# Optimization experiments

Measured on AMD Instinct MI355X. Metric: run time of the kernel, lower is better.

The kernel has to match this reference:

```python
import jax, jax.numpy as jnp
import numpy as np


def setup_inputs() -> dict:
    key = jax.random.key(0)
    kq, kk, kv = jax.random.split(key, 3)
    B, L, S, H, E = 2, 2048, 2048, 16, 64
    queries = jax.random.normal(kq, (B, L, H, E), dtype=jnp.float32)
    keys = jax.random.normal(kk, (B, S, H, E), dtype=jnp.float32)
    values = jax.random.normal(kv, (B, S, H, E), dtype=jnp.float32)
    # TriangularCausalMask: True strictly above the diagonal (positions to mask)
    causal = jnp.triu(jnp.ones((L, S), dtype=jnp.bool_), k=1)
    attn_mask = jnp.broadcast_to(causal[None, None, :, :], (B, 1, L, S))
    return {"queries": queries, "keys": keys, "values": values, "attn_mask": attn_mask}


def reference(queries, keys, values, attn_mask):
    # queries: [B,L,H,E], keys/values: [B,S,H,E], attn_mask: [B,1,L,S] bool
    E = queries.shape[-1]
    scale = 1.0 / jnp.sqrt(jnp.asarray(E, dtype=queries.dtype))
    scores = jnp.einsum('blhe,bshe->bhls', queries, keys)      # [B,H,L,S]
    scores = jnp.where(attn_mask, -jnp.inf, scores)
    A = jax.nn.softmax(scale * scores, axis=-1)                # dropout is identity in eval
    V = jnp.einsum('bhls,bshd->blhd', A, values)               # [B,L,H,D]
    return V, A
```

## Files before the change

kernel.cpp:

```cpp
#include <hip/hip_runtime.h>
#include <hip/hip_bf16.h>


#define B_ 2
#define L_ 2048
#define S_ 2048
#define H_ 16
#define E_ 64
#define HE 1024
#define KP 72
#define PP 68

typedef __attribute__((ext_vector_type(8))) __bf16 bfrag;
typedef __attribute__((ext_vector_type(4))) float f32x4;

__device__ __forceinline__ unsigned short f2bu(float x) {
    __bf16 b = (__bf16)x;
    return __builtin_bit_cast(unsigned short, b);
}

__global__ __launch_bounds__(256, 2)
void fullattn_kernel(const float* __restrict__ Qg,
                     const float* __restrict__ Kg,
                     const float* __restrict__ Vg,
                     float* __restrict__ Vout,
                     float* __restrict__ Aout)
{
    __shared__ __align__(16) __bf16 Ks[64 * KP];
    __shared__ __align__(16) __bf16 Vt[64 * KP];
    __shared__ __align__(16) float  Pw[4][16 * PP];

    const int tid  = threadIdx.x;
    const int wave = tid >> 6;
    const int lane = tid & 63;
    const int ln   = lane & 15;
    const int quad = lane >> 4;
    const int lq   = quad * 4;

    const int qt = blockIdx.x;
    const int bh = blockIdx.y;
    const int b  = bh >> 4;
    const int h  = bh & 15;

    const int q0  = qt * 64;
    const int q0w = q0 + wave * 16;

    const float* qbase = Qg + ((size_t)b * L_ * H_ + h) * E_;
    const float* kbase = Kg + ((size_t)b * S_ * H_ + h) * E_;
    const float* vbase = Vg + ((size_t)b * S_ * H_ + h) * E_;
    float* arow0 = Aout + (size_t)bh * L_ * S_;

    bfrag qf[2];
    {
        const float* qr = qbase + (size_t)(q0w + ln) * HE;
        #pragma unroll
        for (int kc = 0; kc < 2; ++kc) {
            const float* p = qr + kc * 32 + quad * 8;
            float4 a0 = *(const float4*)(p);
            float4 a1 = *(const float4*)(p + 4);
            bfrag f;
            f[0] = (__bf16)(a0.x * 0.125f); f[1] = (__bf16)(a0.y * 0.125f);
            f[2] = (__bf16)(a0.z * 0.125f); f[3] = (__bf16)(a0.w * 0.125f);
            f[4] = (__bf16)(a1.x * 0.125f); f[5] = (__bf16)(a1.y * 0.125f);
            f[6] = (__bf16)(a1.z * 0.125f); f[7] = (__bf16)(a1.w * 0.125f);
            qf[kc] = f;
        }
    }

    const int r  = tid >> 2;
    const int c0 = tid & 3;

    float lsum[4] = {0.f, 0.f, 0.f, 0.f};
    for (int st = 0; st <= qt; ++st) {
        const int s0 = st * 64;
        __syncthreads();
        {
            const float* kr = kbase + (size_t)(s0 + r) * HE;
            #pragma unroll
            for (int i = 0; i < 4; ++i) {
                int f4 = c0 + i * 4;
                float4 kv = *(const float4*)(kr + f4 * 4);
                ushort4 kb;
                kb.x = f2bu(kv.x); kb.y = f2bu(kv.y);
                kb.z = f2bu(kv.z); kb.w = f2bu(kv.w);
                *(ushort4*)&Ks[r * KP + f4 * 4] = kb;
            }
        }
        __syncthreads();
        #pragma unroll
        for (int nc = 0; nc < 4; ++nc) {
            f32x4 acc = {0.f, 0.f, 0.f, 0.f};
            #pragma unroll
            for (int kc = 0; kc < 2; ++kc) {
                bfrag bk = *(const bfrag*)&Ks[(nc * 16 + ln) * KP + kc * 32 + quad * 8];
                acc = __builtin_amdgcn_mfma_f32_16x16x32_bf16(qf[kc], bk, acc, 0, 0, 0);
            }
            const int s_abs = s0 + nc * 16 + ln;
            #pragma unroll
            for (int rg = 0; rg < 4; ++rg) {
                const int q_abs = q0w + lq + rg;
                float e = (s_abs <= q_abs) ? __expf(acc[rg]) : 0.0f;
                lsum[rg] += e;
            }
        }
    }

    float inv_l[4];
    #pragma unroll
    for (int rg = 0; rg < 4; ++rg) {
        float v = lsum[rg];
        v += __shfl_xor(v, 1);
        v += __shfl_xor(v, 2);
        v += __shfl_xor(v, 4);
        v += __shfl_xor(v, 8);
        inv_l[rg] = 1.0f / v;
    }

    f32x4 oacc[4];
    #pragma unroll
    for (int dc = 0; dc < 4; ++dc) {
        f32x4 z = {0.f, 0.f, 0.f, 0.f};
        oacc[dc] = z;
    }

    const int wr = lane >> 2;
    const int wc = (lane & 3) * 4;

    for (int st = 0; st <= qt; ++st) {
        const int s0 = st * 64;
        __syncthreads();
        {
            const float* kr = kbase + (size_t)(s0 + r) * HE;
            const float* vr = vbase + (size_t)(s0 + r) * HE;
            #pragma unroll
            for (int i = 0; i < 4; ++i) {
                int f4 = c0 + i * 4;
                float4 kv = *(const float4*)(kr + f4 * 4);
                float4 vv = *(const float4*)(vr + f4 * 4);
                ushort4 kb;
                kb.x = f2bu(kv.x); kb.y = f2bu(kv.y);
                kb.z = f2bu(kv.z); kb.w = f2bu(kv.w);
                *(ushort4*)&Ks[r * KP + f4 * 4] = kb;
                const int d0 = f4 * 4;
                Vt[(d0 + 0) * KP + r] = (__bf16)vv.x;
                Vt[(d0 + 1) * KP + r] = (__bf16)vv.y;
                Vt[(d0 + 2) * KP + r] = (__bf16)vv.z;
                Vt[(d0 + 3) * KP + r] = (__bf16)vv.w;
            }
        }
        __syncthreads();

        #pragma unroll
        for (int nc = 0; nc < 4; ++nc) {
            f32x4 acc = {0.f, 0.f, 0.f, 0.f};
            #pragma unroll
            for (int kc = 0; kc < 2; ++kc) {
                bfrag bk = *(const bfrag*)&Ks[(nc * 16 + ln) * KP + kc * 32 + quad * 8];
                acc = __builtin_amdgcn_mfma_f32_16x16x32_bf16(qf[kc], bk, acc, 0, 0, 0);
            }
            const int s_abs = s0 + nc * 16 + ln;
            #pragma unroll
            for (int rg = 0; rg < 4; ++rg) {
                const int q_abs = q0w + lq + rg;
                float e = (s_abs <= q_abs) ? __expf(acc[rg]) : 0.0f;
                Pw[wave][(lq + rg) * PP + nc * 16 + ln] = e * inv_l[rg];
            }
        }

        bfrag af[2];
        #pragma unroll
        for (int kc = 0; kc < 2; ++kc) {
            const float* pp = &Pw[wave][ln * PP + kc * 32 + quad * 8];
            float4 p0 = *(const float4*)pp;
            float4 p1 = *(const float4*)(pp + 4);
            bfrag f;
            f[0] = (__bf16)p0.x; f[1] = (__bf16)p0.y;
            f[2] = (__bf16)p0.z; f[3] = (__bf16)p0.w;
            f[4] = (__bf16)p1.x; f[5] = (__bf16)p1.y;
            f[6] = (__bf16)p1.z; f[7] = (__bf16)p1.w;
            af[kc] = f;
        }

        #pragma unroll
        for (int dc = 0; dc < 4; ++dc) {
            #pragma unroll
            for (int kc = 0; kc < 2; ++kc) {
                bfrag bv = *(const bfrag*)&Vt[(dc * 16 + ln) * KP + kc * 32 + quad * 8];
                oacc[dc] = __builtin_amdgcn_mfma_f32_16x16x32_bf16(af[kc], bv, oacc[dc], 0, 0, 0);
            }
        }

        float* ar = arow0 + (size_t)(q0w + wr) * S_ + s0;
        #pragma unroll
        for (int c4 = 0; c4 < 4; ++c4) {
            float4 v4 = *(const float4*)&Pw[wave][wr * PP + wc + c4 * 16];
            *(float4*)(ar + wc + c4 * 16) = v4;
        }
    }

    {
        const float4 z4 = {0.f, 0.f, 0.f, 0.f};
        for (int st = qt + 1; st < S_ / 64; ++st) {
            float* ar = arow0 + (size_t)(q0w + wr) * S_ + st * 64;
            #pragma unroll
            for (int c4 = 0; c4 < 4; ++c4)
                *(float4*)(ar + wc + c4 * 16) = z4;
        }
    }

    #pragma unroll
    for (int rg = 0; rg < 4; ++rg) {
        float* vr = Vout + ((size_t)(b * L_ + q0w + lq + rg) * H_ + h) * E_;
        #pragma unroll
        for (int dc = 0; dc < 4; ++dc)
            vr[dc * 16 + ln] = oacc[dc][rg];
    }
}

extern "C" void kernel_launch(void* const* d_in, const int* in_sizes, int n_in,
                              void* d_out, int out_size, void* d_ws, size_t ws_size,
                              hipStream_t stream) {
    const float* Q = (const float*)d_in[0];
    const float* K = (const float*)d_in[1];
    const float* V = (const float*)d_in[2];
    float* out  = (float*)d_out;
    float* Vo   = out;
    float* Ao   = out + (size_t)B_ * L_ * H_ * E_;
    dim3 grid(L_ / 64, B_ * H_);
    fullattn_kernel<<<grid, 256, 0, stream>>>(Q, K, V, Vo, Ao);
}
```

Before: 729.2 us.

## Split rowsum into separate kernel, register-prefetch K/V tiles, bf16 P staging

Moves the first pass (row sums of exp scores) into its own kernel that writes inverse normalizers to workspace, and the main kernel reads them. Both kernels now prefetch the next K/V tile into registers while computing the current one, and occupancy hints go from 2 to 4 blocks. P is staged in shared memory as bf16, and the A matrix is written straight from registers as scalar stores instead of float4 stores through shared memory. This trades an extra launch, a workspace round trip and less coalesced A writes for more overlap and occupancy.

```diff
diff --git a/kernel.cpp b/kernel.cpp
--- a/kernel.cpp
+++ b/kernel.cpp
@@ -9,7 +9,7 @@
 #define E_ 64
 #define HE 1024
 #define KP 72
-#define PP 68
+#define PWP 72
 
 typedef __attribute__((ext_vector_type(8))) __bf16 bfrag;
 typedef __attribute__((ext_vector_type(4))) float f32x4;
@@ -19,16 +19,12 @@
     return __builtin_bit_cast(unsigned short, b);
 }
 
-__global__ __launch_bounds__(256, 2)
-void fullattn_kernel(const float* __restrict__ Qg,
-                     const float* __restrict__ Kg,
-                     const float* __restrict__ Vg,
-                     float* __restrict__ Vout,
-                     float* __restrict__ Aout)
+__global__ __launch_bounds__(256, 4)
+void rowsum_kernel(const float* __restrict__ Qg,
+                   const float* __restrict__ Kg,
+                   float* __restrict__ invL)
 {
     __shared__ __align__(16) __bf16 Ks[64 * KP];
-    __shared__ __align__(16) __bf16 Vt[64 * KP];
-    __shared__ __align__(16) float  Pw[4][16 * PP];
 
     const int tid  = threadIdx.x;
     const int wave = tid >> 6;
@@ -41,14 +37,10 @@
     const int bh = blockIdx.y;
     const int b  = bh >> 4;
     const int h  = bh & 15;
-
-    const int q0  = qt * 64;
-    const int q0w = q0 + wave * 16;
+    const int q0w = qt * 64 + wave * 16;
 
     const float* qbase = Qg + ((size_t)b * L_ * H_ + h) * E_;
     const float* kbase = Kg + ((size_t)b * S_ * H_ + h) * E_;
-    const float* vbase = Vg + ((size_t)b * S_ * H_ + h) * E_;
-    float* arow0 = Aout + (size_t)bh * L_ * S_;
 
     bfrag qf[2];
     {
@@ -70,23 +62,30 @@
     const int r  = tid >> 2;
     const int c0 = tid & 3;
 
+    float4 kv[4];
+    {
+        const float* kr = kbase + (size_t)r * HE;
+        #pragma unroll
+        for (int i = 0; i < 4; ++i) kv[i] = *(const float4*)(kr + (c0 + i * 4) * 4);
+    }
+
     float lsum[4] = {0.f, 0.f, 0.f, 0.f};
     for (int st = 0; st <= qt; ++st) {
+        __syncthreads();
+        #pragma unroll
+        for (int i = 0; i < 4; ++i) {
+            ushort4 kb;
+            kb.x = f2bu(kv[i].x); kb.y = f2bu(kv[i].y);
+            kb.z = f2bu(kv[i].z); kb.w = f2bu(kv[i].w);
+            *(ushort4*)&Ks[r * KP + (c0 + i * 4) * 4] = kb;
+        }
+        __syncthreads();
+        if (st < qt) {
+            const float* kr = kbase + (size_t)((st + 1) * 64 + r) * HE;
+            #pragma unroll
+            for (int i = 0; i < 4; ++i) kv[i] = *(const float4*)(kr + (c0 + i * 4) * 4);
+        }
         const int s0 = st * 64;
-        __syncthreads();
-        {
-            const float* kr = kbase + (size_t)(s0 + r) * HE;
-            #pragma unroll
-            for (int i = 0; i < 4; ++i) {
-                int f4 = c0 + i * 4;
-                float4 kv = *(const float4*)(kr + f4 * 4);
-                ushort4 kb;
-                kb.x = f2bu(kv.x); kb.y = f2bu(kv.y);
-                kb.z = f2bu(kv.z); kb.w = f2bu(kv.w);
-                *(ushort4*)&Ks[r * KP + f4 * 4] = kb;
-            }
-        }
-        __syncthreads();
         #pragma unroll
         for (int nc = 0; nc < 4; ++nc) {
             f32x4 acc = {0.f, 0.f, 0.f, 0.f};
@@ -99,13 +98,11 @@
             #pragma unroll
             for (int rg = 0; rg < 4; ++rg) {
                 const int q_abs = q0w + lq + rg;
-                float e = (s_abs <= q_abs) ? __expf(acc[rg]) : 0.0f;
-                lsum[rg] += e;
-            }
-        }
-    }
-
-    float inv_l[4];
+                lsum[rg] += (s_abs <= q_abs) ? __expf(acc[rg]) : 0.f;
+            }
+        }
+    }
+
     #pragma unroll
     for (int rg = 0; rg < 4; ++rg) {
         float v = lsum[rg];
@@ -113,8 +110,61 @@
         v += __shfl_xor(v, 2);
         v += __shfl_xor(v, 4);
         v += __shfl_xor(v, 8);
-        inv_l[rg] = 1.0f / v;
-    }
+        if (ln == 0) invL[(size_t)bh * L_ + q0w + lq + rg] = 1.0f / v;
+    }
+}
+
+__global__ __launch_bounds__(256, 4)
+void fullattn_kernel(const float* __restrict__ Qg,
+                     const float* __restrict__ Kg,
+                     const float* __restrict__ Vg,
+                     const float* __restrict__ invL,
+                     float* __restrict__ Vout,
+                     float* __restrict__ Aout)
+{
+    __shared__ __align__(16) __bf16 Ks[64 * KP];
+    __shared__ __align__(16) __bf16 Vt[64 * KP];
+    __shared__ __align__(16) __bf16 Pwb[4][16 * PWP];
+
+    const int tid  = threadIdx.x;
+    const int wave = tid >> 6;
+    const int lane = tid & 63;
+    const int ln   = lane & 15;
+    const int quad = lane >> 4;
+    const int lq   = quad * 4;
+
+    const int qt = blockIdx.x;
+    const int bh = blockIdx.y;
+    const int b  = bh >> 4;
+    const int h  = bh & 15;
+    const int q0w = qt * 64 + wave * 16;
+
+    const float* qbase = Qg + ((size_t)b * L_ * H_ + h) * E_;
+    const float* kbase = Kg + ((size_t)b * S_ * H_ + h) * E_;
+    const float* vbase = Vg + ((size_t)b * S_ * H_ + h) * E_;
+    float* arow0 = Aout + (size_t)bh * L_ * S_;
+
+    bfrag qf[2];
+    {
+        const float* qr = qbase + (size_t)(q0w + ln) * HE;
+        #pragma unroll
+        for (int kc = 0; kc < 2; ++kc) {
+            const float* p = qr + kc * 32 + quad * 8;
+            float4 a0 = *(const float4*)(p);
+            float4 a1 = *(const float4*)(p + 4);
+            bfrag f;
+            f[0] = (__bf16)(a0.x * 0.125f); f[1] = (__bf16)(a0.y * 0.125f);
+            f[2] = (__bf16)(a0.z * 0.125f); f[3] = (__bf16)(a0.w * 0.125f);
+            f[4] = (__bf16)(a1.x * 0.125f); f[5] = (__bf16)(a1.y * 0.125f);
+            f[6] = (__bf16)(a1.z * 0.125f); f[7] = (__bf16)(a1.w * 0.125f);
+            qf[kc] = f;
+        }
+    }
+
+    float inv_l[4];
+    #pragma unroll
+    for (int rg = 0; rg < 4; ++rg)
+        inv_l[rg] = invL[(size_t)bh * L_ + q0w + lq + rg];
 
     f32x4 oacc[4];
     #pragma unroll
@@ -123,32 +173,51 @@
         oacc[dc] = z;
     }
 
-    const int wr = lane >> 2;
-    const int wc = (lane & 3) * 4;
+    const int r  = tid >> 2;
+    const int c0 = tid & 3;
+
+    float4 kv[4], vv[4];
+    {
+        const float* kr = kbase + (size_t)r * HE;
+        const float* vr = vbase + (size_t)r * HE;
+        #pragma unroll
+        for (int i = 0; i < 4; ++i) {
+            kv[i] = *(const float4*)(kr + (c0 + i * 4) * 4);
+            vv[i] = *(const float4*)(vr + (c0 + i * 4) * 4);
+        }
+    }
+
+    float* arp[4];
+    #pragma unroll
+    for (int rg = 0; rg < 4; ++rg)
+        arp[rg] = arow0 + (size_t)(q0w + lq + rg) * S_ + ln;
 
     for (int st = 0; st <= qt; ++st) {
         const int s0 = st * 64;
         __syncthreads();
-        {
-            const float* kr = kbase + (size_t)(s0 + r) * HE;
-            const float* vr = vbase + (size_t)(s0 + r) * HE;
+        #pragma unroll
+        for (int i = 0; i < 4; ++i) {
+            const int f4 = c0 + i * 4;
+            ushort4 kb;
+            kb.x = f2bu(kv[i].x); kb.y = f2bu(kv[i].y);
+            kb.z = f2bu(kv[i].z); kb.w = f2bu(kv[i].w);
+            *(ushort4*)&Ks[r * KP + f4 * 4] = kb;
+            const int d0 = f4 * 4;
+            Vt[(d0 + 0) * KP + r] = (__bf16)vv[i].x;
+            Vt[(d0 + 1) * KP + r] = (__bf16)vv[i].y;
+            Vt[(d0 + 2) * KP + r] = (__bf16)vv[i].z;
+            Vt[(d0 + 3) * KP + r] = (__bf16)vv[i].w;
+        }
+        __syncthreads();
+        if (st < qt) {
+            const float* kr = kbase + (size_t)((st + 1) * 64 + r) * HE;
+            const float* vr = vbase + (size_t)((st + 1) * 64 + r) * HE;
             #pragma unroll
             for (int i = 0; i < 4; ++i) {
-                int f4 = c0 + i * 4;
-                float4 kv = *(const float4*)(kr + f4 * 4);
-                float4 vv = *(const float4*)(vr + f4 * 4);
-                ushort4 kb;
-                kb.x = f2bu(kv.x); kb.y = f2bu(kv.y);
-                kb.z = f2bu(kv.z); kb.w = f2bu(kv.w);
-                *(ushort4*)&Ks[r * KP + f4 * 4] = kb;
-                const int d0 = f4 * 4;
-                Vt[(d0 + 0) * KP + r] = (__bf16)vv.x;
-                Vt[(d0 + 1) * KP + r] = (__bf16)vv.y;
-                Vt[(d0 + 2) * KP + r] = (__bf16)vv.z;
-                Vt[(d0 + 3) * KP + r] = (__bf16)vv.w;
-            }
-        }
-        __syncthreads();
+                kv[i] = *(const float4*)(kr + (c0 + i * 4) * 4);
+                vv[i] = *(const float4*)(vr + (c0 + i * 4) * 4);
+            }
+        }
 
         #pragma unroll
         for (int nc = 0; nc < 4; ++nc) {
@@ -162,24 +231,17 @@
             #pragma unroll
             for (int rg = 0; rg < 4; ++rg) {
                 const int q_abs = q0w + lq + rg;
-                float e = (s_abs <= q_abs) ? __expf(acc[rg]) : 0.0f;
-                Pw[wave][(lq + rg) * PP + nc * 16 + ln] = e * inv_l[rg];
+                float e = (s_abs <= q_abs) ? __expf(acc[rg]) : 0.f;
+                float p = e * inv_l[rg];
+                arp[rg][s0 + nc * 16] = p;
+                Pwb[wave][(lq + rg) * PWP + nc * 16 + ln] = (__bf16)p;
             }
         }
 
         bfrag af[2];
         #pragma unroll
-        for (int kc = 0; kc < 2; ++kc) {
-            const float* pp = &Pw[wave][ln * PP + kc * 32 + quad * 8];
-            float4 p0 = *(const float4*)pp;
-            float4 p1 = *(const float4*)(pp + 4);
-            bfrag f;
-            f[0] = (__bf16)p0.x; f[1] = (__bf16)p0.y;
-            f[2] = (__bf16)p0.z; f[3] = (__bf16)p0.w;
-            f[4] = (__bf16)p1.x; f[5] = (__bf16)p1.y;
-            f[6] = (__bf16)p1.z; f[7] = (__bf16)p1.w;
-            af[kc] = f;
-        }
+        for (int kc = 0; kc < 2; ++kc)
+            af[kc] = *(const bfrag*)&Pwb[wave][ln * PWP + kc * 32 + quad * 8];
 
         #pragma unroll
         for (int dc = 0; dc < 4; ++dc) {
@@ -189,16 +251,11 @@
                 oacc[dc] = __builtin_amdgcn_mfma_f32_16x16x32_bf16(af[kc], bv, oacc[dc], 0, 0, 0);
             }
         }
-
-        float* ar = arow0 + (size_t)(q0w + wr) * S_ + s0;
-        #pragma unroll
-        for (int c4 = 0; c4 < 4; ++c4) {
-            float4 v4 = *(const float4*)&Pw[wave][wr * PP + wc + c4 * 16];
-            *(float4*)(ar + wc + c4 * 16) = v4;
-        }
-    }
-
-    {
+    }
+
+    {
+        const int wr = lane >> 2;
+        const int wc = (lane & 3) * 4;
         const float4 z4 = {0.f, 0.f, 0.f, 0.f};
         for (int st = qt + 1; st < S_ / 64; ++st) {
             float* ar = arow0 + (size_t)(q0w + wr) * S_ + st * 64;
@@ -226,6 +283,9 @@
     float* out  = (float*)d_out;
     float* Vo   = out;
     float* Ao   = out + (size_t)B_ * L_ * H_ * E_;
+    float* invL = (float*)d_ws;
+
     dim3 grid(L_ / 64, B_ * H_);
-    fullattn_kernel<<<grid, 256, 0, stream>>>(Q, K, V, Vo, Ao);
-}
+    rowsum_kernel<<<grid, 256, 0, stream>>>(Q, K, invL);
+    fullattn_kernel<<<grid, 256, 0, stream>>>(Q, K, V, invL, Vo, Ao);
+}
```

Result: slower. 745.9 us (+2.3%).
